# Optimization experiments

Hardware: AMD Instinct MI355X
Metric: run time of the kernel (lower is better)

Reference implementation:

```python
import jax, jax.numpy as jnp
import numpy as np


def setup_inputs() -> dict:
    key = jax.random.key(0)
    k1, k2, k3, k4 = jax.random.split(key, 4)
    n1, n2, d, num_types = 8192, 8192, 512, 64
    return {
        "input1": jax.random.normal(k1, (n1, d), dtype=jnp.float32),
        "input2": jax.random.normal(k2, (n2, d), dtype=jnp.float32),
        "weight": jax.random.normal(k3, (num_types, d), dtype=jnp.float32),
        "bias": jax.random.uniform(k4, (1,), dtype=jnp.float32),
        "type_index": 3,
    }


def reference(input1, input2, weight, bias, type_index):
    # DistMult score: (input1 * w_r) @ input2^T + bias.
    # Original builds diag(w_r) and does a dense d x d GEMM; the faithful
    # math is an elementwise row-scale followed by one GEMM.
    w_r = weight[type_index]                      # [d]
    scaled = input1 * w_r[None, :]                # [n1, d]
    out = scaled @ input2.T + bias                # [n1, n2]
    return out  # act is identity
```

## Files before the change

### kernel.cpp

```cpp
#include <hip/hip_runtime.h>


#define N1 8192
#define N2 8192
#define DK 512
#define BM 128
#define BN 128
#define BK 64

typedef short bf16x8 __attribute__((ext_vector_type(8)));
typedef float f32x4 __attribute__((ext_vector_type(4)));

__device__ __forceinline__ unsigned short f2bf(float f) {
    unsigned int u = __float_as_uint(f);
    u = (u + 0x7FFFu + ((u >> 16) & 1u)) >> 16;
    return (unsigned short)u;
}

__global__ __launch_bounds__(256) void convert_kernel(
        const float* __restrict__ in1, const float* __restrict__ in2,
        const float* __restrict__ weight, const int* __restrict__ type_index,
        unsigned short* __restrict__ a_bf, unsigned short* __restrict__ b_bf) {
    const int QA = N1 * DK / 4;
    int i = blockIdx.x * blockDim.x + threadIdx.x;
    if (i < QA) {
        float4 v = reinterpret_cast<const float4*>(in1)[i];
        int c4 = i & (DK / 4 - 1);
        float4 w = reinterpret_cast<const float4*>(weight + (size_t)(*type_index) * DK)[c4];
        ushort4 o;
        o.x = f2bf(v.x * w.x);
        o.y = f2bf(v.y * w.y);
        o.z = f2bf(v.z * w.z);
        o.w = f2bf(v.w * w.w);
        reinterpret_cast<ushort4*>(a_bf)[i] = o;
    } else {
        int j = i - QA;
        float4 v = reinterpret_cast<const float4*>(in2)[j];
        ushort4 o;
        o.x = f2bf(v.x);
        o.y = f2bf(v.y);
        o.z = f2bf(v.z);
        o.w = f2bf(v.w);
        reinterpret_cast<ushort4*>(b_bf)[j] = o;
    }
}

__global__ __launch_bounds__(256) void gemm_bt(
        const unsigned short* __restrict__ A, const unsigned short* __restrict__ B,
        const float* __restrict__ bias, float* __restrict__ C) {
    __shared__ __align__(16) unsigned short ldsA[BM * BK];
    __shared__ __align__(16) unsigned short ldsB[BN * BK];

    const int tid  = threadIdx.x;
    const int wave = tid >> 6;
    const int lane = tid & 63;
    const int quad = lane >> 4;
    const int r16  = lane & 15;
    const int wm   = wave & 1;
    const int wn   = wave >> 1;

    const int bm = blockIdx.y * BM;
    const int bn = blockIdx.x * BN;

    f32x4 acc[4][4];
#pragma unroll
    for (int i = 0; i < 4; ++i)
#pragma unroll
        for (int j = 0; j < 4; ++j)
            acc[i][j] = (f32x4){0.f, 0.f, 0.f, 0.f};

    const int l8   = lane >> 3;
    const int perm = (lane & 7) ^ l8;
    const int srow = wave * 32 + l8;
    const int scol = perm * 8;
    const unsigned short* ag = A + (size_t)(bm + srow) * DK + scol;
    const unsigned short* bg = B + (size_t)(bn + srow) * DK + scol;
    unsigned short* la = &ldsA[wave * 2048];
    unsigned short* lb = &ldsB[wave * 2048];

    const int rs   = r16 & 7;
    const int col0 = ((0 * 4 + quad) ^ rs) * 8;
    const int col1 = ((1 * 4 + quad) ^ rs) * 8;

    for (int kt = 0; kt < DK; kt += BK) {
#pragma unroll
        for (int i = 0; i < 4; ++i) {
            __builtin_amdgcn_global_load_lds(ag + kt + i * 8 * DK, la + i * 512, 16, 0, 0);
            __builtin_amdgcn_global_load_lds(bg + kt + i * 8 * DK, lb + i * 512, 16, 0, 0);
        }
        __syncthreads();

        {
            bf16x8 af[4], bfr[4];
#pragma unroll
            for (int mi = 0; mi < 4; ++mi)
                af[mi] = *(const bf16x8*)&ldsA[(wm * 64 + mi * 16 + r16) * BK + col0];
#pragma unroll
            for (int ni = 0; ni < 4; ++ni)
                bfr[ni] = *(const bf16x8*)&ldsB[(wn * 64 + ni * 16 + r16) * BK + col0];
#pragma unroll
            for (int mi = 0; mi < 4; ++mi)
#pragma unroll
                for (int ni = 0; ni < 4; ++ni)
                    acc[mi][ni] = __builtin_amdgcn_mfma_f32_16x16x32_bf16(
                        af[mi], bfr[ni], acc[mi][ni], 0, 0, 0);
        }
        {
            bf16x8 af[4], bfr[4];
#pragma unroll
            for (int mi = 0; mi < 4; ++mi)
                af[mi] = *(const bf16x8*)&ldsA[(wm * 64 + mi * 16 + r16) * BK + col1];
#pragma unroll
            for (int ni = 0; ni < 4; ++ni)
                bfr[ni] = *(const bf16x8*)&ldsB[(wn * 64 + ni * 16 + r16) * BK + col1];
#pragma unroll
            for (int mi = 0; mi < 4; ++mi)
#pragma unroll
                for (int ni = 0; ni < 4; ++ni)
                    acc[mi][ni] = __builtin_amdgcn_mfma_f32_16x16x32_bf16(
                        af[mi], bfr[ni], acc[mi][ni], 0, 0, 0);
        }
        __syncthreads();
    }

    const float bv = bias[0];
#pragma unroll
    for (int mi = 0; mi < 4; ++mi) {
        const int row0 = bm + wm * 64 + mi * 16 + quad * 4;
#pragma unroll
        for (int ni = 0; ni < 4; ++ni) {
            const int col = bn + wn * 64 + ni * 16 + r16;
#pragma unroll
            for (int r = 0; r < 4; ++r)
                C[(size_t)(row0 + r) * N2 + col] = acc[mi][ni][r] + bv;
        }
    }
}

__global__ void naive_kernel(const float* __restrict__ in1, const float* __restrict__ in2,
                             const float* __restrict__ weight, const int* __restrict__ type_index,
                             const float* __restrict__ bias, float* __restrict__ out) {
    int col = blockIdx.x * 16 + threadIdx.x;
    int row = blockIdx.y * 16 + threadIdx.y;
    const float* wr = weight + (size_t)(*type_index) * DK;
    float s = 0.f;
    for (int k = 0; k < DK; ++k)
        s += in1[(size_t)row * DK + k] * wr[k] * in2[(size_t)col * DK + k];
    out[(size_t)row * N2 + col] = s + bias[0];
}

extern "C" void kernel_launch(void* const* d_in, const int* in_sizes, int n_in,
                              void* d_out, int out_size, void* d_ws, size_t ws_size,
                              hipStream_t stream) {
    const float* in1  = (const float*)d_in[0];
    const float* in2  = (const float*)d_in[1];
    const float* wgt  = (const float*)d_in[2];
    const float* bias = (const float*)d_in[3];
    const int*   tix  = (const int*)d_in[4];
    float* out = (float*)d_out;

    const size_t need = 2ull * (N1 + N2) * DK;
    if (ws_size >= need) {
        unsigned short* a_bf = (unsigned short*)d_ws;
        unsigned short* b_bf = a_bf + (size_t)N1 * DK;

        const int total4 = (N1 + N2) * DK / 4;
        convert_kernel<<<total4 / 256, 256, 0, stream>>>(in1, in2, wgt, tix, a_bf, b_bf);

        dim3 grid(N2 / BN, N1 / BM);
        gemm_bt<<<grid, 256, 0, stream>>>(a_bf, b_bf, bias, out);
    } else {
        dim3 grid(N2 / 16, N1 / 16);
        dim3 blk(16, 16);
        naive_kernel<<<grid, blk, 0, stream>>>(in1, in2, wgt, tix, bias, out);
    }
}
```

Before: 340.1 us.

## Add 256x256 double-buffered GEMM kernel with 512 threads and prefetch

Adds a new GEMM kernel that uses 256x256 output tiles, 8 waves and 128KB of dynamic LDS. The LDS is double-buffered so the next K-slab is loaded with global_load_lds while MFMAs run on the current one, synchronised with explicit vmcnt waits and barriers. Larger tiles cut global and LDS traffic per FLOP, and the prefetch is meant to hide load latency. In exchange the kernel runs one block per CU with high register pressure, and the grid shrinks to 1024 blocks, which may leave tail imbalance.

```diff
diff --git a/kernel.cpp b/kernel.cpp
--- a/kernel.cpp
+++ b/kernel.cpp
@@ -4,12 +4,15 @@
 #define N1 8192
 #define N2 8192
 #define DK 512
-#define BM 128
-#define BN 128
 #define BK 64
+#define NT (DK / BK)
 
 typedef short bf16x8 __attribute__((ext_vector_type(8)));
 typedef float f32x4 __attribute__((ext_vector_type(4)));
+
+#define FENCE() asm volatile("" ::: "memory")
+#define VMC(n)  asm volatile("s_waitcnt vmcnt(" #n ")" ::: "memory")
+#define BARR()  do { FENCE(); __builtin_amdgcn_s_barrier(); FENCE(); } while (0)
 
 __device__ __forceinline__ unsigned short f2bf(float f) {
     unsigned int u = __float_as_uint(f);
@@ -45,11 +48,120 @@
     }
 }
 
+__global__ __launch_bounds__(512, 1) void gemm_256(
+        const unsigned short* __restrict__ A, const unsigned short* __restrict__ B,
+        const float* __restrict__ bias, float* __restrict__ C) {
+    extern __shared__ char sm[];
+    const int tid  = threadIdx.x;
+    const int wave = tid >> 6;
+    const int lane = tid & 63;
+    const int quad = lane >> 4;
+    const int r16  = lane & 15;
+    const int wm   = wave >> 2;
+    const int wn   = wave & 3;
+
+    const int bm = blockIdx.y * 256;
+    const int bn = blockIdx.x * 256;
+
+    f32x4 acc[8][4];
+#pragma unroll
+    for (int i = 0; i < 8; ++i)
+#pragma unroll
+        for (int j = 0; j < 4; ++j)
+            acc[i][j] = (f32x4){0.f, 0.f, 0.f, 0.f};
+
+    const int l8   = lane >> 3;
+    const int perm = (lane & 7) ^ l8;
+    const unsigned short* ag = A + (size_t)(bm + wave * 32 + l8) * DK + perm * 8;
+    const unsigned short* bg = B + (size_t)(bn + wave * 32 + l8) * DK + perm * 8;
+    const int wbase = wave * 4096;
+
+    const int rs   = r16 & 7;
+    const int col0 = ((0 * 4 + quad) ^ rs) * 16;
+    const int col1 = ((1 * 4 + quad) ^ rs) * 16;
+    const int rowA = (wm * 128 + r16) * 128;
+    const int rowB = (wn * 64  + r16) * 128;
+
+#define STAGE(T, BUF) do {                                                        \
+    char* dA = sm + (BUF) * 32768 + wbase;                                        \
+    char* dB = sm + 65536 + (BUF) * 32768 + wbase;                                \
+    _Pragma("unroll") for (int i_ = 0; i_ < 4; ++i_) {                            \
+        __builtin_amdgcn_global_load_lds(ag + (T) * BK + i_ * 8 * DK,             \
+            (unsigned short*)(dA + i_ * 1024), 16, 0, 0);                         \
+        __builtin_amdgcn_global_load_lds(bg + (T) * BK + i_ * 8 * DK,             \
+            (unsigned short*)(dB + i_ * 1024), 16, 0, 0);                         \
+    }                                                                             \
+} while (0)
+
+    STAGE(0, 0);
+
+#pragma unroll 1
+    for (int t = 0; t < NT; ++t) {
+        const int cur = t & 1;
+        if (t + 1 < NT) {
+            STAGE(t + 1, cur ^ 1);
+            VMC(8);
+        } else {
+            VMC(0);
+        }
+        BARR();
+
+        const char* bufA = sm + cur * 32768;
+        const char* bufB = sm + 65536 + cur * 32768;
+
+        {
+            bf16x8 af[8], bfr[4];
+#pragma unroll
+            for (int mi = 0; mi < 8; ++mi)
+                af[mi] = *(const bf16x8*)(bufA + rowA + mi * 2048 + col0);
+#pragma unroll
+            for (int ni = 0; ni < 4; ++ni)
+                bfr[ni] = *(const bf16x8*)(bufB + rowB + ni * 2048 + col0);
+#pragma unroll
+            for (int mi = 0; mi < 8; ++mi)
+#pragma unroll
+                for (int ni = 0; ni < 4; ++ni)
+                    acc[mi][ni] = __builtin_amdgcn_mfma_f32_16x16x32_bf16(
+                        af[mi], bfr[ni], acc[mi][ni], 0, 0, 0);
+        }
+        {
+            bf16x8 af[8], bfr[4];
+#pragma unroll
+            for (int mi = 0; mi < 8; ++mi)
+                af[mi] = *(const bf16x8*)(bufA + rowA + mi * 2048 + col1);
+#pragma unroll
+            for (int ni = 0; ni < 4; ++ni)
+                bfr[ni] = *(const bf16x8*)(bufB + rowB + ni * 2048 + col1);
+#pragma unroll
+            for (int mi = 0; mi < 8; ++mi)
+#pragma unroll
+                for (int ni = 0; ni < 4; ++ni)
+                    acc[mi][ni] = __builtin_amdgcn_mfma_f32_16x16x32_bf16(
+                        af[mi], bfr[ni], acc[mi][ni], 0, 0, 0);
+        }
+        BARR();
+    }
+#undef STAGE
+
+    const float bv = bias[0];
+#pragma unroll
+    for (int mi = 0; mi < 8; ++mi) {
+        const int row0 = bm + wm * 128 + mi * 16 + quad * 4;
+#pragma unroll
+        for (int ni = 0; ni < 4; ++ni) {
+            const int col = bn + wn * 64 + ni * 16 + r16;
+#pragma unroll
+            for (int r = 0; r < 4; ++r)
+                C[(size_t)(row0 + r) * N2 + col] = acc[mi][ni][r] + bv;
+        }
+    }
+}
+
 __global__ __launch_bounds__(256) void gemm_bt(
         const unsigned short* __restrict__ A, const unsigned short* __restrict__ B,
         const float* __restrict__ bias, float* __restrict__ C) {
-    __shared__ __align__(16) unsigned short ldsA[BM * BK];
-    __shared__ __align__(16) unsigned short ldsB[BN * BK];
+    __shared__ __align__(16) unsigned short ldsA[128 * BK];
+    __shared__ __align__(16) unsigned short ldsB[128 * BK];
 
     const int tid  = threadIdx.x;
     const int wave = tid >> 6;
@@ -59,8 +171,8 @@
     const int wm   = wave & 1;
     const int wn   = wave >> 1;
 
-    const int bm = blockIdx.y * BM;
-    const int bn = blockIdx.x * BN;
+    const int bm = blockIdx.y * 128;
+    const int bn = blockIdx.x * 128;
 
     f32x4 acc[4][4];
 #pragma unroll
@@ -167,8 +279,15 @@
         const int total4 = (N1 + N2) * DK / 4;
         convert_kernel<<<total4 / 256, 256, 0, stream>>>(in1, in2, wgt, tix, a_bf, b_bf);
 
-        dim3 grid(N2 / BN, N1 / BM);
-        gemm_bt<<<grid, 256, 0, stream>>>(a_bf, b_bf, bias, out);
+        hipError_t e = hipFuncSetAttribute(
+            reinterpret_cast<const void*>(gemm_256),
+            hipFuncAttributeMaxDynamicSharedMemorySize, 131072);
+        if (e == hipSuccess) {
+            gemm_256<<<dim3(N2 / 256, N1 / 256), 512, 131072, stream>>>(
+                a_bf, b_bf, bias, out);
+        } else {
+            gemm_bt<<<dim3(N2 / 128, N1 / 128), 256, 0, stream>>>(a_bf, b_bf, bias, out);
+        }
     } else {
         dim3 grid(N2 / 16, N1 / 16);
         dim3 blk(16, 16);
```

Result: slower. 378.7 us (+11.3%).
